# Optimization experiments

Hardware: AMD Instinct MI355X
Metric: run time of the kernel (lower is better)

## Reference

```python
import jax, jax.numpy as jnp
import numpy as np

NEG_INF = -1.0e9


def setup_inputs() -> dict:
    key = jax.random.key(0)
    k1, k2, k3, k4 = jax.random.split(key, 4)
    B, N, F, U, H = 4, 2048, 128, 64, 4
    x = jax.random.normal(k1, (B, N, F), dtype=jnp.float32)
    adj = jax.random.randint(k2, (B, N, N), 0, 2, dtype=jnp.int32)
    W = jax.random.normal(k3, (H, F, U), dtype=jnp.float32) * (1.0 / np.sqrt(F))
    b = jnp.zeros((H, U), dtype=jnp.float32)
    a_w = jax.random.normal(k4, (H, U), dtype=jnp.float32) * (1.0 / np.sqrt(U))
    a_b = jnp.zeros((H,), dtype=jnp.float32)
    return {"x": x, "adj": adj, "W": W, "b": b, "a_w": a_w, "a_b": a_b}


def reference(x, adj, W, b, a_w, a_b):
    # Per-head Dense + relu, batched over heads: proj [H,B,N,U]
    proj = jax.nn.relu(jnp.einsum('bnf,hfu->hbnu', x, W) + b[:, None, None, :])
    # Scalar attention score per node: s [H,B,N]
    s = jnp.einsum('hbnu,hu->hbn', proj, a_w) + a_b[:, None, None]
    # Outer-product logits [H,B,N,N], masked by adjacency
    logits = s[:, :, :, None] * s[:, :, None, :]
    logits = jnp.where(adj[None] > 0, logits, NEG_INF)
    scores = jax.nn.softmax(logits, axis=-1)
    # Weighted aggregation, then mean over heads -> [B,N,U]
    out = jnp.einsum('hbij,hbju->hbiu', scores, proj)
    return jnp.mean(out, axis=0)
```

## Files before the change

kernel.cpp:

```cpp
#include <hip/hip_runtime.h>
#include <hip/hip_bf16.h>


#define Bdim 4
#define Ndim 2048
#define Fdim 128
#define Udim 64
#define Hdim 4
#define JC 4
#define JCHUNK (Ndim / JC)

typedef __attribute__((ext_vector_type(8))) short short8;
typedef __attribute__((ext_vector_type(4))) float f32x4;

__device__ __forceinline__ short bf16_rne(float f) {
  union { __hip_bfloat16 b; unsigned short u; } c;
  c.b = __float2bfloat16(f);
  return (short)c.u;
}

__device__ __forceinline__ void splitbf(float f, short& hi, short& lo) {
  unsigned u = __float_as_uint(f);
  hi = (short)(u >> 16);
  float lof = f - __uint_as_float(u & 0xffff0000u);
  lo = bf16_rne(lof);
}

__device__ __forceinline__ void stage16(const void* g, void* l) {
  __builtin_amdgcn_global_load_lds(
      (const __attribute__((address_space(1))) unsigned int*)g,
      (__attribute__((address_space(3))) unsigned int*)l, 16, 0, 0);
}

__global__ __launch_bounds__(256) void pack_adj_kernel(
    const int* __restrict__ adj, unsigned long long* __restrict__ bits,
    int nchunks) {
  const int lane = threadIdx.x & 63;
  const int wid = (blockIdx.x * 256 + threadIdx.x) >> 6;
  const int nw = (gridDim.x * 256) >> 6;
  for (int c = wid * 4; c + 3 < nchunks; c += nw * 4) {
    int v0 = adj[(size_t)(c + 0) * 64 + lane];
    int v1 = adj[(size_t)(c + 1) * 64 + lane];
    int v2 = adj[(size_t)(c + 2) * 64 + lane];
    int v3 = adj[(size_t)(c + 3) * 64 + lane];
    unsigned long long m0 = __ballot(v0 != 0);
    unsigned long long m1 = __ballot(v1 != 0);
    unsigned long long m2 = __ballot(v2 != 0);
    unsigned long long m3 = __ballot(v3 != 0);
    if (lane == 0) {
      bits[c + 0] = m0;
      bits[c + 1] = m1;
      bits[c + 2] = m2;
      bits[c + 3] = m3;
    }
  }
}

__global__ __launch_bounds__(256) void proj_kernel(
    const float* __restrict__ x, const float* __restrict__ W,
    const float* __restrict__ bias, const float* __restrict__ a_w,
    const float* __restrict__ a_b, unsigned short* __restrict__ pTh,
    unsigned short* __restrict__ pTl, float* __restrict__ s) {
  const int bid = blockIdx.x;
  const int nt = bid & 31;
  const int b = (bid >> 5) & 3;
  const int h = bid >> 7;
  const int n0 = nt * 64;

  __shared__ __align__(16) char smem[71168];
  float (*Wl)[Udim] = (float(*)[Udim])(smem);
  float (*xl)[Fdim + 4] = (float(*)[Fdim + 4])(smem + 32768);
  float (*pt)[68] = (float(*)[68])(smem + 32768);
  float* bl = (float*)(smem + 66560);
  float* awl = (float*)(smem + 66816);
  float (*sred)[16] = (float(*)[16])(smem + 67072);

  const int t = threadIdx.x;

  const float* Wg = W + (size_t)h * Fdim * Udim;
  for (int k = t; k < Fdim * Udim / 4; k += 256) {
    ((float4*)&Wl[0][0])[k] = ((const float4*)Wg)[k];
  }
  if (t < Udim) {
    bl[t] = bias[h * Udim + t];
    awl[t] = a_w[h * Udim + t];
  }
  const float* xg = x + ((size_t)b * Ndim + n0) * Fdim;
  for (int k = t; k < 64 * Fdim / 4; k += 256) {
    int row = k >> 5;
    int c4 = k & 31;
    float4 v = ((const float4*)xg)[(size_t)row * (Fdim / 4) + c4];
    *(float4*)&xl[row][c4 * 4] = v;
  }
  __syncthreads();

  const int ug = t & 15, rg = t >> 4;
  const int u0 = ug * 4, r0 = rg * 4;
  float acc[4][4] = {};

#pragma unroll 4
  for (int f = 0; f < Fdim; ++f) {
    const float4 wv = *(const float4*)&Wl[f][u0];
    const float xv[4] = {xl[r0][f], xl[r0 + 1][f], xl[r0 + 2][f], xl[r0 + 3][f]};
#pragma unroll
    for (int c = 0; c < 4; ++c) {
      acc[c][0] = fmaf(xv[c], wv.x, acc[c][0]);
      acc[c][1] = fmaf(xv[c], wv.y, acc[c][1]);
      acc[c][2] = fmaf(xv[c], wv.z, acc[c][2]);
      acc[c][3] = fmaf(xv[c], wv.w, acc[c][3]);
    }
  }

  float po[4][4];
#pragma unroll
  for (int c = 0; c < 4; ++c)
#pragma unroll
    for (int k = 0; k < 4; ++k)
      po[c][k] = fmaxf(acc[c][k] + bl[u0 + k], 0.f);

#pragma unroll
  for (int c = 0; c < 4; ++c) {
    float sp = po[c][0] * awl[u0 + 0] + po[c][1] * awl[u0 + 1] +
               po[c][2] * awl[u0 + 2] + po[c][3] * awl[u0 + 3];
    sred[r0 + c][ug] = sp;
  }
  __syncthreads();

#pragma unroll
  for (int k = 0; k < 4; ++k) {
    float4 v = {po[0][k], po[1][k], po[2][k], po[3][k]};
    *(float4*)&pt[u0 + k][r0] = v;
  }
  __syncthreads();

  const size_t hb = (size_t)h * Bdim + b;
  const int su = t >> 2;
  const int snl = (t & 3) * 16;
  float v[16];
#pragma unroll
  for (int j = 0; j < 4; ++j)
    *(float4*)&v[4 * j] = *(const float4*)&pt[su][snl + 4 * j];
  short hi[16], lo[16];
#pragma unroll
  for (int k = 0; k < 16; ++k) splitbf(v[k], hi[k], lo[k]);
  unsigned short* ph =
      pTh + hb * (size_t)(Udim * Ndim) + (size_t)su * Ndim + n0 + snl;
  unsigned short* pl =
      pTl + hb * (size_t)(Udim * Ndim) + (size_t)su * Ndim + n0 + snl;
  *(short8*)(ph + 0) = *(short8*)&hi[0];
  *(short8*)(ph + 8) = *(short8*)&hi[8];
  *(short8*)(pl + 0) = *(short8*)&lo[0];
  *(short8*)(pl + 8) = *(short8*)&lo[8];

  if (t < 64) {
    float sum = a_b[h];
#pragma unroll
    for (int k = 0; k < 16; ++k) sum += sred[t][k];
    s[hb * Ndim + n0 + t] = sum;
  }
}

__global__ __launch_bounds__(256, 7) void attn_mfma_kernel(
    const unsigned short* __restrict__ pTh,
    const unsigned short* __restrict__ pTl, const float* __restrict__ s,
    const unsigned int* __restrict__ abits, float* __restrict__ out_part,
    float* __restrict__ Z_part) {
  const int bid = blockIdx.x;
  const int jc = bid & 3;
  const int it = (bid >> 2) & 31;
  const int b = (bid >> 7) & 3;
  const int h = bid >> 9;
  const int i0g = it * 64;
  const int j0g = jc * JCHUNK;

  __shared__ float sj[JCHUNK];
  __shared__ unsigned int ab[64][16];
  __shared__ __align__(16) short Bst[2][8][512];

  const int t = threadIdx.x;
  const int wv = t >> 6;
  const int lane = t & 63;
  const int q = lane >> 4;
  const int li = lane & 15;
  const size_t hb = (size_t)h * Bdim + b;
  const float* sg = s + hb * Ndim;

  ((float2*)sj)[t] = ((const float2*)(sg + j0g))[t];
  {
    const int row = t >> 2, w4 = (t & 3) * 4;
    *(uint4*)&ab[row][w4] = *(const uint4*)&abits[((size_t)b * Ndim + i0g +
                                                   row) * (Ndim / 32) +
                                                  (j0g >> 5) + w4];
  }
  const int irow = wv * 16 + li;

  const unsigned short* bsrc_h =
      pTh + hb * (size_t)(Udim * Ndim) + (size_t)(wv * 16 + li) * Ndim + j0g +
      q * 8;
  const unsigned short* bsrc_l =
      pTl + hb * (size_t)(Udim * Ndim) + (size_t)(wv * 16 + li) * Ndim + j0g +
      q * 8;

  stage16(bsrc_h, &Bst[0][wv * 2 + 0][0]);
  stage16(bsrc_l, &Bst[0][wv * 2 + 1][0]);

  f32x4 acc[4] = {};
  float zacc = 0.f;
  __syncthreads();

  const float si = sg[i0g + irow];
  int buf = 0;

  for (int js = 0; js < JCHUNK; js += 32) {
    if (js + 32 < JCHUNK) {
      stage16(bsrc_h + js + 32, &Bst[buf ^ 1][wv * 2 + 0][0]);
      stage16(bsrc_l + js + 32, &Bst[buf ^ 1][wv * 2 + 1][0]);
    }
    const short8 b0h = *(const short8*)&Bst[buf][0][lane * 8];
    const short8 b0l = *(const short8*)&Bst[buf][1][lane * 8];
    const short8 b1h = *(const short8*)&Bst[buf][2][lane * 8];
    const short8 b1l = *(const short8*)&Bst[buf][3][lane * 8];
    const short8 b2h = *(const short8*)&Bst[buf][4][lane * 8];
    const short8 b2l = *(const short8*)&Bst[buf][5][lane * 8];
    const short8 b3h = *(const short8*)&Bst[buf][6][lane * 8];
    const short8 b3l = *(const short8*)&Bst[buf][7][lane * 8];
    const unsigned int mb = (ab[irow][js >> 5] >> (q * 8)) & 0xffu;
    const f32x4 s0 = *(const f32x4*)&sj[js + q * 8];
    const f32x4 s1 = *(const f32x4*)&sj[js + q * 8 + 4];
    const float sv[8] = {s0.x, s0.y, s0.z, s0.w, s1.x, s1.y, s1.z, s1.w};
    short8 ahi, alo;
#pragma unroll
    for (int e = 0; e < 8; ++e) {
      float we = __expf(si * sv[e]);
      we = ((mb >> e) & 1u) ? we : 0.f;
      zacc += we;
      short hh, ll;
      splitbf(we, hh, ll);
      ahi[e] = hh;
      alo[e] = ll;
    }
    acc[0] = __builtin_amdgcn_mfma_f32_16x16x32_bf16(ahi, b0h, acc[0], 0, 0, 0);
    acc[1] = __builtin_amdgcn_mfma_f32_16x16x32_bf16(ahi, b1h, acc[1], 0, 0, 0);
    acc[2] = __builtin_amdgcn_mfma_f32_16x16x32_bf16(ahi, b2h, acc[2], 0, 0, 0);
    acc[3] = __builtin_amdgcn_mfma_f32_16x16x32_bf16(ahi, b3h, acc[3], 0, 0, 0);
    acc[0] = __builtin_amdgcn_mfma_f32_16x16x32_bf16(alo, b0h, acc[0], 0, 0, 0);
    acc[1] = __builtin_amdgcn_mfma_f32_16x16x32_bf16(alo, b1h, acc[1], 0, 0, 0);
    acc[2] = __builtin_amdgcn_mfma_f32_16x16x32_bf16(alo, b2h, acc[2], 0, 0, 0);
    acc[3] = __builtin_amdgcn_mfma_f32_16x16x32_bf16(alo, b3h, acc[3], 0, 0, 0);
    acc[0] = __builtin_amdgcn_mfma_f32_16x16x32_bf16(ahi, b0l, acc[0], 0, 0, 0);
    acc[1] = __builtin_amdgcn_mfma_f32_16x16x32_bf16(ahi, b1l, acc[1], 0, 0, 0);
    acc[2] = __builtin_amdgcn_mfma_f32_16x16x32_bf16(ahi, b2l, acc[2], 0, 0, 0);
    acc[3] = __builtin_amdgcn_mfma_f32_16x16x32_bf16(ahi, b3l, acc[3], 0, 0, 0);
    __syncthreads();
    buf ^= 1;
  }

  zacc += __shfl_xor(zacc, 16, 64);
  zacc += __shfl_xor(zacc, 32, 64);
  const size_t pslab = ((size_t)h * JC + jc) * Bdim + b;
  if (q == 0) Z_part[pslab * Ndim + i0g + wv * 16 + li] = zacc;

  float* cbuf = (float*)&Bst[0][0][0];
#pragma unroll
  for (int r = 0; r < 4; ++r)
#pragma unroll
    for (int m = 0; m < 4; ++m)
      cbuf[wv * 1024 + (q * 4 + r) * 64 + m * 16 + li] = acc[m][r];
  __syncthreads();
  {
    const int row = lane >> 2, c0 = (lane & 3) * 16;
    const float* src = &cbuf[wv * 1024 + row * 64 + c0];
    float* op =
        out_part + (pslab * Ndim + i0g + wv * 16 + row) * Udim + c0;
#pragma unroll
    for (int k = 0; k < 4; ++k)
      *(float4*)(op + k * 4) = *(const float4*)(src + k * 4);
  }
}

__global__ __launch_bounds__(256) void combine_kernel(
    const float* __restrict__ out_part, const float* __restrict__ Z_part,
    float* __restrict__ out) {
  const int idx = blockIdx.x * 256 + threadIdx.x;
  const int u4 = idx & 15;
  const size_t bn = (size_t)(idx >> 4);
  float4 r = {0.f, 0.f, 0.f, 0.f};
#pragma unroll
  for (int h = 0; h < Hdim; ++h) {
    float4 p = {0.f, 0.f, 0.f, 0.f};
    float z = 0.f;
#pragma unroll
    for (int j = 0; j < JC; ++j) {
      const size_t sl = ((size_t)h * JC + j) * (Bdim * Ndim) + bn;
      float4 pj = ((const float4*)out_part)[sl * (Udim / 4) + u4];
      p.x += pj.x; p.y += pj.y; p.z += pj.z; p.w += pj.w;
      z += Z_part[sl];
    }
    z = (z != 0.f) ? z : 1.f;
    const float inv = 1.f / z;
    r.x += p.x * inv;
    r.y += p.y * inv;
    r.z += p.z * inv;
    r.w += p.w * inv;
  }
  r.x *= 0.25f; r.y *= 0.25f; r.z *= 0.25f; r.w *= 0.25f;
  ((float4*)out)[idx] = r;
}

extern "C" void kernel_launch(void* const* d_in, const int* in_sizes, int n_in,
                              void* d_out, int out_size, void* d_ws,
                              size_t ws_size, hipStream_t stream) {
  const float* x = (const float*)d_in[0];
  const int* adj = (const int*)d_in[1];
  const float* W = (const float*)d_in[2];
  const float* bias = (const float*)d_in[3];
  const float* a_w = (const float*)d_in[4];
  const float* a_b = (const float*)d_in[5];
  float* out = (float*)d_out;

  char* ws = (char*)d_ws;
  unsigned short* pTh = (unsigned short*)(ws + 0);
  unsigned short* pTl = (unsigned short*)(ws + 4194304);
  float* s = (float*)(ws + 8388608);
  unsigned int* adjbits = (unsigned int*)(ws + 8519680);
  float* out_part = (float*)(ws + 10616832);
  float* Z_part = (float*)(ws + 44171264);

  const int nchunks = Bdim * Ndim * Ndim / 64;
  pack_adj_kernel<<<2048, 256, 0, stream>>>(adj, (unsigned long long*)adjbits,
                                            nchunks);
  proj_kernel<<<Hdim * Bdim * 32, 256, 0, stream>>>(x, W, bias, a_w, a_b, pTh,
                                                    pTl, s);
  attn_mfma_kernel<<<Hdim * Bdim * 32 * JC, 256, 0, stream>>>(
      pTh, pTl, s, adjbits, out_part, Z_part);
  combine_kernel<<<(Bdim * Ndim * Udim / 4) / 256, 256, 0, stream>>>(
      out_part, Z_part, out);
}
```

Before: 171.4 us.

## Halve j-split, widen stage to 64 columns, raise MFMA priority, store directly

The column split is reduced from four chunks to two, so each block processes a 1024-wide j range. The staging step now loads 64 columns per barrier instead of 32, and the MFMA chains are wrapped in s_setprio. The LDS-transposed output store is replaced with direct scattered global stores, and the Z_part offset is moved to match the smaller partial buffer. This cuts partial-sum traffic, barrier count and combine work, at the cost of half as many blocks, more LDS per block, lower occupancy and less coalesced output writes.

```diff
diff --git a/kernel.cpp b/kernel.cpp
--- a/kernel.cpp
+++ b/kernel.cpp
@@ -7,8 +7,9 @@
 #define Fdim 128
 #define Udim 64
 #define Hdim 4
-#define JC 4
+#define JC 2
 #define JCHUNK (Ndim / JC)
+#define JSUB 64
 
 typedef __attribute__((ext_vector_type(8))) short short8;
 typedef __attribute__((ext_vector_type(4))) float f32x4;
@@ -160,22 +161,22 @@
   }
 }
 
-__global__ __launch_bounds__(256, 7) void attn_mfma_kernel(
+__global__ __launch_bounds__(256, 3) void attn_mfma_kernel(
     const unsigned short* __restrict__ pTh,
     const unsigned short* __restrict__ pTl, const float* __restrict__ s,
     const unsigned int* __restrict__ abits, float* __restrict__ out_part,
     float* __restrict__ Z_part) {
   const int bid = blockIdx.x;
-  const int jc = bid & 3;
-  const int it = (bid >> 2) & 31;
-  const int b = (bid >> 7) & 3;
-  const int h = bid >> 9;
+  const int jc = bid & 1;
+  const int it = (bid >> 1) & 31;
+  const int b = (bid >> 6) & 3;
+  const int h = bid >> 8;
   const int i0g = it * 64;
   const int j0g = jc * JCHUNK;
 
   __shared__ float sj[JCHUNK];
-  __shared__ unsigned int ab[64][16];
-  __shared__ __align__(16) short Bst[2][8][512];
+  __shared__ unsigned int ab[64][33];
+  __shared__ __align__(16) short Bst[2][8][1024];
 
   const int t = threadIdx.x;
   const int wv = t >> 6;
@@ -185,12 +186,11 @@
   const size_t hb = (size_t)h * Bdim + b;
   const float* sg = s + hb * Ndim;
 
-  ((float2*)sj)[t] = ((const float2*)(sg + j0g))[t];
-  {
-    const int row = t >> 2, w4 = (t & 3) * 4;
-    *(uint4*)&ab[row][w4] = *(const uint4*)&abits[((size_t)b * Ndim + i0g +
-                                                   row) * (Ndim / 32) +
-                                                  (j0g >> 5) + w4];
+  ((float4*)sj)[t] = ((const float4*)(sg + j0g))[t];
+  for (int k = t; k < 64 * 32; k += 256) {
+    int row = k >> 5, w = k & 31;
+    ab[row][w] =
+        abits[((size_t)b * Ndim + i0g + row) * (Ndim / 32) + (j0g >> 5) + w];
   }
   const int irow = wv * 16 + li;
 
@@ -201,8 +201,10 @@
       pTl + hb * (size_t)(Udim * Ndim) + (size_t)(wv * 16 + li) * Ndim + j0g +
       q * 8;
 
-  stage16(bsrc_h, &Bst[0][wv * 2 + 0][0]);
-  stage16(bsrc_l, &Bst[0][wv * 2 + 1][0]);
+  stage16(bsrc_h + 0, &Bst[0][wv * 2 + 0][0]);
+  stage16(bsrc_h + 32, &Bst[0][wv * 2 + 0][512]);
+  stage16(bsrc_l + 0, &Bst[0][wv * 2 + 1][0]);
+  stage16(bsrc_l + 32, &Bst[0][wv * 2 + 1][512]);
 
   f32x4 acc[4] = {};
   float zacc = 0.f;
@@ -211,46 +213,55 @@
   const float si = sg[i0g + irow];
   int buf = 0;
 
-  for (int js = 0; js < JCHUNK; js += 32) {
-    if (js + 32 < JCHUNK) {
-      stage16(bsrc_h + js + 32, &Bst[buf ^ 1][wv * 2 + 0][0]);
-      stage16(bsrc_l + js + 32, &Bst[buf ^ 1][wv * 2 + 1][0]);
-    }
-    const short8 b0h = *(const short8*)&Bst[buf][0][lane * 8];
-    const short8 b0l = *(const short8*)&Bst[buf][1][lane * 8];
-    const short8 b1h = *(const short8*)&Bst[buf][2][lane * 8];
-    const short8 b1l = *(const short8*)&Bst[buf][3][lane * 8];
-    const short8 b2h = *(const short8*)&Bst[buf][4][lane * 8];
-    const short8 b2l = *(const short8*)&Bst[buf][5][lane * 8];
-    const short8 b3h = *(const short8*)&Bst[buf][6][lane * 8];
-    const short8 b3l = *(const short8*)&Bst[buf][7][lane * 8];
-    const unsigned int mb = (ab[irow][js >> 5] >> (q * 8)) & 0xffu;
-    const f32x4 s0 = *(const f32x4*)&sj[js + q * 8];
-    const f32x4 s1 = *(const f32x4*)&sj[js + q * 8 + 4];
-    const float sv[8] = {s0.x, s0.y, s0.z, s0.w, s1.x, s1.y, s1.z, s1.w};
-    short8 ahi, alo;
-#pragma unroll
-    for (int e = 0; e < 8; ++e) {
-      float we = __expf(si * sv[e]);
-      we = ((mb >> e) & 1u) ? we : 0.f;
-      zacc += we;
-      short hh, ll;
-      splitbf(we, hh, ll);
-      ahi[e] = hh;
-      alo[e] = ll;
-    }
-    acc[0] = __builtin_amdgcn_mfma_f32_16x16x32_bf16(ahi, b0h, acc[0], 0, 0, 0);
-    acc[1] = __builtin_amdgcn_mfma_f32_16x16x32_bf16(ahi, b1h, acc[1], 0, 0, 0);
-    acc[2] = __builtin_amdgcn_mfma_f32_16x16x32_bf16(ahi, b2h, acc[2], 0, 0, 0);
-    acc[3] = __builtin_amdgcn_mfma_f32_16x16x32_bf16(ahi, b3h, acc[3], 0, 0, 0);
-    acc[0] = __builtin_amdgcn_mfma_f32_16x16x32_bf16(alo, b0h, acc[0], 0, 0, 0);
-    acc[1] = __builtin_amdgcn_mfma_f32_16x16x32_bf16(alo, b1h, acc[1], 0, 0, 0);
-    acc[2] = __builtin_amdgcn_mfma_f32_16x16x32_bf16(alo, b2h, acc[2], 0, 0, 0);
-    acc[3] = __builtin_amdgcn_mfma_f32_16x16x32_bf16(alo, b3h, acc[3], 0, 0, 0);
-    acc[0] = __builtin_amdgcn_mfma_f32_16x16x32_bf16(ahi, b0l, acc[0], 0, 0, 0);
-    acc[1] = __builtin_amdgcn_mfma_f32_16x16x32_bf16(ahi, b1l, acc[1], 0, 0, 0);
-    acc[2] = __builtin_amdgcn_mfma_f32_16x16x32_bf16(ahi, b2l, acc[2], 0, 0, 0);
-    acc[3] = __builtin_amdgcn_mfma_f32_16x16x32_bf16(ahi, b3l, acc[3], 0, 0, 0);
+  for (int js = 0; js < JCHUNK; js += JSUB) {
+    if (js + JSUB < JCHUNK) {
+      stage16(bsrc_h + js + 64, &Bst[buf ^ 1][wv * 2 + 0][0]);
+      stage16(bsrc_h + js + 96, &Bst[buf ^ 1][wv * 2 + 0][512]);
+      stage16(bsrc_l + js + 64, &Bst[buf ^ 1][wv * 2 + 1][0]);
+      stage16(bsrc_l + js + 96, &Bst[buf ^ 1][wv * 2 + 1][512]);
+    }
+    const unsigned int w0 = ab[irow][(js >> 5) + 0];
+    const unsigned int w1 = ab[irow][(js >> 5) + 1];
+#pragma unroll
+    for (int g = 0; g < 2; ++g) {
+      const unsigned int mb = ((g ? w1 : w0) >> (q * 8)) & 0xffu;
+      const f32x4 s0 = *(const f32x4*)&sj[js + g * 32 + q * 8];
+      const f32x4 s1 = *(const f32x4*)&sj[js + g * 32 + q * 8 + 4];
+      const float sv[8] = {s0.x, s0.y, s0.z, s0.w, s1.x, s1.y, s1.z, s1.w};
+      short8 ahi, alo;
+#pragma unroll
+      for (int e = 0; e < 8; ++e) {
+        float we = __expf(si * sv[e]);
+        we = ((mb >> e) & 1u) ? we : 0.f;
+        zacc += we;
+        short hh, ll;
+        splitbf(we, hh, ll);
+        ahi[e] = hh;
+        alo[e] = ll;
+      }
+      const short8 b0h = *(const short8*)&Bst[buf][0][g * 512 + lane * 8];
+      const short8 b0l = *(const short8*)&Bst[buf][1][g * 512 + lane * 8];
+      const short8 b1h = *(const short8*)&Bst[buf][2][g * 512 + lane * 8];
+      const short8 b1l = *(const short8*)&Bst[buf][3][g * 512 + lane * 8];
+      const short8 b2h = *(const short8*)&Bst[buf][4][g * 512 + lane * 8];
+      const short8 b2l = *(const short8*)&Bst[buf][5][g * 512 + lane * 8];
+      const short8 b3h = *(const short8*)&Bst[buf][6][g * 512 + lane * 8];
+      const short8 b3l = *(const short8*)&Bst[buf][7][g * 512 + lane * 8];
+      __builtin_amdgcn_s_setprio(1);
+      acc[0] = __builtin_amdgcn_mfma_f32_16x16x32_bf16(ahi, b0h, acc[0], 0, 0, 0);
+      acc[1] = __builtin_amdgcn_mfma_f32_16x16x32_bf16(ahi, b1h, acc[1], 0, 0, 0);
+      acc[2] = __builtin_amdgcn_mfma_f32_16x16x32_bf16(ahi, b2h, acc[2], 0, 0, 0);
+      acc[3] = __builtin_amdgcn_mfma_f32_16x16x32_bf16(ahi, b3h, acc[3], 0, 0, 0);
+      acc[0] = __builtin_amdgcn_mfma_f32_16x16x32_bf16(alo, b0h, acc[0], 0, 0, 0);
+      acc[1] = __builtin_amdgcn_mfma_f32_16x16x32_bf16(alo, b1h, acc[1], 0, 0, 0);
+      acc[2] = __builtin_amdgcn_mfma_f32_16x16x32_bf16(alo, b2h, acc[2], 0, 0, 0);
+      acc[3] = __builtin_amdgcn_mfma_f32_16x16x32_bf16(alo, b3h, acc[3], 0, 0, 0);
+      acc[0] = __builtin_amdgcn_mfma_f32_16x16x32_bf16(ahi, b0l, acc[0], 0, 0, 0);
+      acc[1] = __builtin_amdgcn_mfma_f32_16x16x32_bf16(ahi, b1l, acc[1], 0, 0, 0);
+      acc[2] = __builtin_amdgcn_mfma_f32_16x16x32_bf16(ahi, b2l, acc[2], 0, 0, 0);
+      acc[3] = __builtin_amdgcn_mfma_f32_16x16x32_bf16(ahi, b3l, acc[3], 0, 0, 0);
+      __builtin_amdgcn_s_setprio(0);
+    }
     __syncthreads();
     buf ^= 1;
   }
@@ -260,21 +271,14 @@
   const size_t pslab = ((size_t)h * JC + jc) * Bdim + b;
   if (q == 0) Z_part[pslab * Ndim + i0g + wv * 16 + li] = zacc;
 
-  float* cbuf = (float*)&Bst[0][0][0];
-#pragma unroll
-  for (int r = 0; r < 4; ++r)
-#pragma unroll
-    for (int m = 0; m < 4; ++m)
-      cbuf[wv * 1024 + (q * 4 + r) * 64 + m * 16 + li] = acc[m][r];
-  __syncthreads();
-  {
-    const int row = lane >> 2, c0 = (lane & 3) * 16;
-    const float* src = &cbuf[wv * 1024 + row * 64 + c0];
-    float* op =
-        out_part + (pslab * Ndim + i0g + wv * 16 + row) * Udim + c0;
-#pragma unroll
-    for (int k = 0; k < 4; ++k)
-      *(float4*)(op + k * 4) = *(const float4*)(src + k * 4);
+  float* op = out_part + (pslab * Ndim + i0g + wv * 16) * Udim;
+#pragma unroll
+  for (int r = 0; r < 4; ++r) {
+    const int ir = q * 4 + r;
+#pragma unroll
+    for (int m = 0; m < 4; ++m) {
+      op[(size_t)ir * Udim + m * 16 + li] = acc[m][r];
+    }
   }
 }
 
@@ -324,7 +328,7 @@
   float* s = (float*)(ws + 8388608);
   unsigned int* adjbits = (unsigned int*)(ws + 8519680);
   float* out_part = (float*)(ws + 10616832);
-  float* Z_part = (float*)(ws + 44171264);
+  float* Z_part = (float*)(ws + 27394048);
 
   const int nchunks = Bdim * Ndim * Ndim / 64;
   pack_adj_kernel<<<2048, 256, 0, stream>>>(adj, (unsigned long long*)adjbits,
```

Result: no change. 173.1 us (+1.0%).

## Unroll attention loop by two with static LDS buffers, setprio, and padded layouts

Applied to the files above, without the earlier changes.

Unrolls the main j-loop by two with fixed double buffers in a manually carved shared memory block, so the staging of the next tile is issued before the current step's compute. It moves the exp and bf16-split work ahead of the LDS B reads and wraps the MFMA block in s_setprio to favour matrix issue. The adjacency bit table and output staging buffer are padded (17 and 68 strides) to avoid bank conflicts. The post-accumulation __syncthreads is dropped because each wave writes and reads only its own cbuf slice, though that slice overlaps sj/ab. Occupancy hint lowers from 7 to 6 blocks per CU.

```diff
diff --git a/kernel.cpp b/kernel.cpp
--- a/kernel.cpp
+++ b/kernel.cpp
@@ -160,7 +160,47 @@
   }
 }
 
-__global__ __launch_bounds__(256, 7) void attn_mfma_kernel(
+#define ASTEP(BBASE, JS)                                                       \
+  do {                                                                         \
+    const unsigned int mb = (ab[irow][(JS) >> 5] >> (q * 8)) & 0xffu;          \
+    const f32x4 s0 = *(const f32x4*)&sj[(JS) + q * 8];                         \
+    const f32x4 s1 = *(const f32x4*)&sj[(JS) + q * 8 + 4];                     \
+    const float sv[8] = {s0.x, s0.y, s0.z, s0.w, s1.x, s1.y, s1.z, s1.w};      \
+    short8 ahi, alo;                                                           \
+    _Pragma("unroll") for (int e = 0; e < 8; ++e) {                            \
+      float we = __expf(si * sv[e]);                                           \
+      we = ((mb >> e) & 1u) ? we : 0.f;                                        \
+      zacc += we;                                                              \
+      short hh, ll;                                                            \
+      splitbf(we, hh, ll);                                                     \
+      ahi[e] = hh;                                                             \
+      alo[e] = ll;                                                             \
+    }                                                                          \
+    const short8 b0h = *(const short8*)((BBASE) + 0 * 512 + lane * 8);         \
+    const short8 b0l = *(const short8*)((BBASE) + 1 * 512 + lane * 8);         \
+    const short8 b1h = *(const short8*)((BBASE) + 2 * 512 + lane * 8);         \
+    const short8 b1l = *(const short8*)((BBASE) + 3 * 512 + lane * 8);         \
+    const short8 b2h = *(const short8*)((BBASE) + 4 * 512 + lane * 8);         \
+    const short8 b2l = *(const short8*)((BBASE) + 5 * 512 + lane * 8);         \
+    const short8 b3h = *(const short8*)((BBASE) + 6 * 512 + lane * 8);         \
+    const short8 b3l = *(const short8*)((BBASE) + 7 * 512 + lane * 8);         \
+    __builtin_amdgcn_s_setprio(1);                                             \
+    acc[0] = __builtin_amdgcn_mfma_f32_16x16x32_bf16(ahi, b0h, acc[0],0,0,0);  \
+    acc[1] = __builtin_amdgcn_mfma_f32_16x16x32_bf16(ahi, b1h, acc[1],0,0,0);  \
+    acc[2] = __builtin_amdgcn_mfma_f32_16x16x32_bf16(ahi, b2h, acc[2],0,0,0);  \
+    acc[3] = __builtin_amdgcn_mfma_f32_16x16x32_bf16(ahi, b3h, acc[3],0,0,0);  \
+    acc[0] = __builtin_amdgcn_mfma_f32_16x16x32_bf16(alo, b0h, acc[0],0,0,0);  \
+    acc[1] = __builtin_amdgcn_mfma_f32_16x16x32_bf16(alo, b1h, acc[1],0,0,0);  \
+    acc[2] = __builtin_amdgcn_mfma_f32_16x16x32_bf16(alo, b2h, acc[2],0,0,0);  \
+    acc[3] = __builtin_amdgcn_mfma_f32_16x16x32_bf16(alo, b3h, acc[3],0,0,0);  \
+    acc[0] = __builtin_amdgcn_mfma_f32_16x16x32_bf16(ahi, b0l, acc[0],0,0,0);  \
+    acc[1] = __builtin_amdgcn_mfma_f32_16x16x32_bf16(ahi, b1l, acc[1],0,0,0);  \
+    acc[2] = __builtin_amdgcn_mfma_f32_16x16x32_bf16(ahi, b2l, acc[2],0,0,0);  \
+    acc[3] = __builtin_amdgcn_mfma_f32_16x16x32_bf16(ahi, b3l, acc[3],0,0,0);  \
+    __builtin_amdgcn_s_setprio(0);                                             \
+  } while (0)
+
+__global__ __launch_bounds__(256, 6) void attn_mfma_kernel(
     const unsigned short* __restrict__ pTh,
     const unsigned short* __restrict__ pTl, const float* __restrict__ s,
     const unsigned int* __restrict__ abits, float* __restrict__ out_part,
@@ -173,9 +213,12 @@
   const int i0g = it * 64;
   const int j0g = jc * JCHUNK;
 
-  __shared__ float sj[JCHUNK];
-  __shared__ unsigned int ab[64][16];
-  __shared__ __align__(16) short Bst[2][8][512];
+  __shared__ __align__(16) char smem[22784];
+  float* sj = (float*)smem;
+  unsigned int (*ab)[17] = (unsigned int(*)[17])(smem + 2048);
+  short* Bst0 = (short*)(smem + 6400);
+  short* Bst1 = (short*)(smem + 14592);
+  float* cbuf = (float*)smem;
 
   const int t = threadIdx.x;
   const int wv = t >> 6;
@@ -187,10 +230,14 @@
 
   ((float2*)sj)[t] = ((const float2*)(sg + j0g))[t];
   {
-    const int row = t >> 2, w4 = (t & 3) * 4;
-    *(uint4*)&ab[row][w4] = *(const uint4*)&abits[((size_t)b * Ndim + i0g +
-                                                   row) * (Ndim / 32) +
-                                                  (j0g >> 5) + w4];
+    const int row = t >> 2, w0 = (t & 3) * 4;
+    uint4 v = *(const uint4*)&abits[((size_t)b * Ndim + i0g + row) *
+                                        (Ndim / 32) +
+                                    jc * 16 + w0];
+    ab[row][w0 + 0] = v.x;
+    ab[row][w0 + 1] = v.y;
+    ab[row][w0 + 2] = v.z;
+    ab[row][w0 + 3] = v.w;
   }
   const int irow = wv * 16 + li;
 
@@ -201,58 +248,26 @@
       pTl + hb * (size_t)(Udim * Ndim) + (size_t)(wv * 16 + li) * Ndim + j0g +
       q * 8;
 
-  stage16(bsrc_h, &Bst[0][wv * 2 + 0][0]);
-  stage16(bsrc_l, &Bst[0][wv * 2 + 1][0]);
+  stage16(bsrc_h, Bst0 + (wv * 2 + 0) * 512);
+  stage16(bsrc_l, Bst0 + (wv * 2 + 1) * 512);
 
   f32x4 acc[4] = {};
   float zacc = 0.f;
   __syncthreads();
 
   const float si = sg[i0g + irow];
-  int buf = 0;
-
-  for (int js = 0; js < JCHUNK; js += 32) {
-    if (js + 32 < JCHUNK) {
-      stage16(bsrc_h + js + 32, &Bst[buf ^ 1][wv * 2 + 0][0]);
-      stage16(bsrc_l + js + 32, &Bst[buf ^ 1][wv * 2 + 1][0]);
+
+  for (int js = 0; js < JCHUNK; js += 64) {
+    stage16(bsrc_h + js + 32, Bst1 + (wv * 2 + 0) * 512);
+    stage16(bsrc_l + js + 32, Bst1 + (wv * 2 + 1) * 512);
+    ASTEP(Bst0, js);
+    __syncthreads();
+    if (js + 64 < JCHUNK) {
+      stage16(bsrc_h + js + 64, Bst0 + (wv * 2 + 0) * 512);
+      stage16(bsrc_l + js + 64, Bst0 + (wv * 2 + 1) * 512);
     }
-    const short8 b0h = *(const short8*)&Bst[buf][0][lane * 8];
-    const short8 b0l = *(const short8*)&Bst[buf][1][lane * 8];
-    const short8 b1h = *(const short8*)&Bst[buf][2][lane * 8];
-    const short8 b1l = *(const short8*)&Bst[buf][3][lane * 8];
-    const short8 b2h = *(const short8*)&Bst[buf][4][lane * 8];
-    const short8 b2l = *(const short8*)&Bst[buf][5][lane * 8];
-    const short8 b3h = *(const short8*)&Bst[buf][6][lane * 8];
-    const short8 b3l = *(const short8*)&Bst[buf][7][lane * 8];
-    const unsigned int mb = (ab[irow][js >> 5] >> (q * 8)) & 0xffu;
-    const f32x4 s0 = *(const f32x4*)&sj[js + q * 8];
-    const f32x4 s1 = *(const f32x4*)&sj[js + q * 8 + 4];
-    const float sv[8] = {s0.x, s0.y, s0.z, s0.w, s1.x, s1.y, s1.z, s1.w};
-    short8 ahi, alo;
-#pragma unroll
-    for (int e = 0; e < 8; ++e) {
-      float we = __expf(si * sv[e]);
-      we = ((mb >> e) & 1u) ? we : 0.f;
-      zacc += we;
-      short hh, ll;
-      splitbf(we, hh, ll);
-      ahi[e] = hh;
-      alo[e] = ll;
-    }
-    acc[0] = __builtin_amdgcn_mfma_f32_16x16x32_bf16(ahi, b0h, acc[0], 0, 0, 0);
-    acc[1] = __builtin_amdgcn_mfma_f32_16x16x32_bf16(ahi, b1h, acc[1], 0, 0, 0);
-    acc[2] = __builtin_amdgcn_mfma_f32_16x16x32_bf16(ahi, b2h, acc[2], 0, 0, 0);
-    acc[3] = __builtin_amdgcn_mfma_f32_16x16x32_bf16(ahi, b3h, acc[3], 0, 0, 0);
-    acc[0] = __builtin_amdgcn_mfma_f32_16x16x32_bf16(alo, b0h, acc[0], 0, 0, 0);
-    acc[1] = __builtin_amdgcn_mfma_f32_16x16x32_bf16(alo, b1h, acc[1], 0, 0, 0);
-    acc[2] = __builtin_amdgcn_mfma_f32_16x16x32_bf16(alo, b2h, acc[2], 0, 0, 0);
-    acc[3] = __builtin_amdgcn_mfma_f32_16x16x32_bf16(alo, b3h, acc[3], 0, 0, 0);
-    acc[0] = __builtin_amdgcn_mfma_f32_16x16x32_bf16(ahi, b0l, acc[0], 0, 0, 0);
-    acc[1] = __builtin_amdgcn_mfma_f32_16x16x32_bf16(ahi, b1l, acc[1], 0, 0, 0);
-    acc[2] = __builtin_amdgcn_mfma_f32_16x16x32_bf16(ahi, b2l, acc[2], 0, 0, 0);
-    acc[3] = __builtin_amdgcn_mfma_f32_16x16x32_bf16(ahi, b3l, acc[3], 0, 0, 0);
+    ASTEP(Bst1, js + 32);
     __syncthreads();
-    buf ^= 1;
   }
 
   zacc += __shfl_xor(zacc, 16, 64);
@@ -260,18 +275,16 @@
   const size_t pslab = ((size_t)h * JC + jc) * Bdim + b;
   if (q == 0) Z_part[pslab * Ndim + i0g + wv * 16 + li] = zacc;
 
-  float* cbuf = (float*)&Bst[0][0][0];
+  float* cb = cbuf + wv * 16 * 68;
 #pragma unroll
   for (int r = 0; r < 4; ++r)
 #pragma unroll
     for (int m = 0; m < 4; ++m)
-      cbuf[wv * 1024 + (q * 4 + r) * 64 + m * 16 + li] = acc[m][r];
-  __syncthreads();
+      cb[(q * 4 + r) * 68 + m * 16 + li] = acc[m][r];
   {
     const int row = lane >> 2, c0 = (lane & 3) * 16;
-    const float* src = &cbuf[wv * 1024 + row * 64 + c0];
-    float* op =
-        out_part + (pslab * Ndim + i0g + wv * 16 + row) * Udim + c0;
+    const float* src = cb + row * 68 + c0;
+    float* op = out_part + (pslab * Ndim + i0g + wv * 16 + row) * Udim + c0;
 #pragma unroll
     for (int k = 0; k < 4; ++k)
       *(float4*)(op + k * 4) = *(const float4*)(src + k * 4);
```

Measured after the change: 178.8 us. 1.04x slower.
